# Optimization experiments

Measured on AMD Instinct MI355X. Metric: run time of the kernel, lower is better.

The kernel has to match this reference:

```python
import jax, jax.numpy as jnp
import numpy as np

N_NODES = 50000
N_EDGES = 800000
HIDDEN = 128
CONTEXT = 128


def setup_inputs() -> dict:
    key = jax.random.key(0)
    ks = jax.random.split(key, 8)
    s = 1.0 / np.sqrt(HIDDEN)
    return {
        "x": jax.random.normal(ks[0], (N_NODES, HIDDEN), jnp.float32),
        "edge_index": jax.random.randint(ks[1], (2, N_EDGES), 0, N_NODES, jnp.int64),
        "W_le": jax.random.normal(ks[2], (HIDDEN, 1), jnp.float32) * s,
        "b_le": jnp.zeros((1,), jnp.float32),
        "W1": jax.random.normal(ks[3], (HIDDEN, HIDDEN), jnp.float32) * s,
        "b1": jnp.zeros((HIDDEN,), jnp.float32),
        "W2": jax.random.normal(ks[4], (HIDDEN, CONTEXT), jnp.float32) * s,
        "b2": jnp.zeros((CONTEXT,), jnp.float32),
    }


def reference(x, edge_index, W_le, b_le, W1, b1, W2, b2):
    N = x.shape[0]
    src, dst = edge_index[0], edge_index[1]
    ar = jnp.arange(N)

    # leader election logits [N]
    logits = (x @ W_le + b_le)[:, 0]

    # extended edges with self loops (every destination segment non-empty)
    ext_src = jnp.concatenate([src, ar])
    ext_dst = jnp.concatenate([dst, ar])

    # scatter_max of source logits onto destinations; recover winning SOURCE node index
    val = logits[ext_src]                                   # [E+N]
    seg_max = jax.ops.segment_max(val, ext_dst, num_segments=N)  # [N]
    winner = jnp.where(val == seg_max[ext_dst], ext_src, -1)
    leader_idx = jax.ops.segment_max(winner, ext_dst, num_segments=N)  # [N] int
    is_leader = ar == leader_idx                            # [N] bool

    # scatter_mean of neighbor features onto destinations
    nsum = jax.ops.segment_sum(x[src], dst, num_segments=N)            # [N, H]
    cnt = jax.ops.segment_sum(jnp.ones((src.shape[0],), x.dtype), dst, num_segments=N)
    nmean = nsum / jnp.maximum(cnt, 1.0)[:, None]

    # squad report MLP (exact GELU, matching torch nn.GELU default)
    h = jax.nn.gelu(nmean @ W1 + b1, approximate=False)
    reports = h @ W2 + b2                                   # [N, C]
    all_reports = jnp.where(is_leader[:, None], reports, 0.0)

    # each node reads its leader's report
    squad_context = all_reports[leader_idx]                 # [N, C]
    return squad_context
```

## Files before the change

### kernel.cpp

```cpp
#include <hip/hip_runtime.h>
#include <stdint.h>

constexpr int NN  = 50000;
constexpr int NE  = 800000;
constexpr int H   = 128;
constexpr int CAP = 48;
constexpr int RB  = 8;

__device__ __forceinline__ uint32_t f32key(float f) {
  uint32_t b = __float_as_uint(f);
  return (b & 0x80000000u) ? ~b : (b | 0x80000000u);
}

__global__ void k_logits(const float* __restrict__ x,
                         const float* __restrict__ Wle, const float* __restrict__ ble,
                         float* __restrict__ logits, unsigned long long* __restrict__ lkey,
                         int* __restrict__ cnt, int* __restrict__ nsl) {
  int gid  = blockIdx.x * blockDim.x + threadIdx.x;
  int wave = gid >> 6, lane = threadIdx.x & 63;
  if (gid == 0) *nsl = 0;
  if (wave >= NN) return;
  const float* xr = x + (size_t)wave * H;
  float v = xr[lane] * Wle[lane] + xr[lane + 64] * Wle[lane + 64];
  for (int off = 32; off > 0; off >>= 1) v += __shfl_xor(v, off, 64);
  if (lane == 0) {
    float lg = v + ble[0];
    logits[wave] = lg;
    lkey[wave] = ((unsigned long long)f32key(lg) << 32) | (unsigned long long)(uint32_t)wave;
    cnt[wave] = 0;
  }
}

__global__ void k_elect(const int* __restrict__ esrc, const int* __restrict__ edst,
                        const float* __restrict__ logits, unsigned long long* __restrict__ lkey) {
  int e = blockIdx.x * blockDim.x + threadIdx.x;
  if (e >= NE) return;
  int s = __builtin_nontemporal_load(&esrc[e]);
  int d = __builtin_nontemporal_load(&edst[e]);
  unsigned long long key =
      ((unsigned long long)f32key(logits[s]) << 32) | (unsigned long long)(uint32_t)s;
  atomicMax(&lkey[d], key);
}

__global__ void k_place(const int* __restrict__ esrc, const int* __restrict__ edst,
                        const unsigned long long* __restrict__ lkey,
                        int* __restrict__ cnt, int* __restrict__ bucket,
                        int* __restrict__ slist, int* __restrict__ nsl) {
  const int* __restrict__ leader_lo = (const int*)lkey;
  int t = blockIdx.x * blockDim.x + threadIdx.x;
  if (t < NN) {
    if (leader_lo[2 * t] == t) {
      int p = atomicAdd(nsl, 1);
      slist[p] = t;
    }
  }
  if (t >= NE) return;
  int d = __builtin_nontemporal_load(&edst[t]);
  if (leader_lo[2 * d] != d) return;
  int s = esrc[t];
  int slot = atomicAdd(&cnt[d], 1);
  if (slot < CAP) bucket[(size_t)d * CAP + slot] = s;
}

__global__ void __launch_bounds__(256) k_report(
    const int* __restrict__ slist, const int* __restrict__ nsl,
    const int* __restrict__ cnt, const int* __restrict__ bucket,
    const float* __restrict__ x,
    const float* __restrict__ W1, const float* __restrict__ b1,
    const float* __restrict__ W2, const float* __restrict__ b2,
    float* __restrict__ out) {
  int base = blockIdx.x * RB;
  int ns = *nsl;
  if (base >= ns) return;
  int v = min(RB, ns - base);

  __shared__ float sm[RB][H];
  __shared__ float hm[RB][H];
  __shared__ int   ss[RB][CAP];
  __shared__ int   nodes[RB];
  __shared__ int   craw[RB];

  int tid = threadIdx.x;
  int j = tid & 127, half = tid >> 7;

  if (tid < RB) {
    int node = slist[base + min(tid, v - 1)];
    nodes[tid] = node;
    craw[tid] = cnt[node];
  }
  __syncthreads();
  for (int r = half; r < v; r += 2) {
    int cc = min(craw[r], CAP);
    if (j < cc) ss[r][j] = bucket[(size_t)nodes[r] * CAP + j];
  }
  __syncthreads();
  for (int rp = 0; rp < RB / 2; ++rp) {
    int r = 2 * rp + half;
    if (r >= v) break;
    int c = craw[r], cc = min(c, CAP);
    double a0 = 0.0, a1 = 0.0;
    int e = 0;
    for (; e + 1 < cc; e += 2) {
      a0 += (double)x[(size_t)ss[r][e] * H + j];
      a1 += (double)x[(size_t)ss[r][e + 1] * H + j];
    }
    if (e < cc) a0 += (double)x[(size_t)ss[r][e] * H + j];
    sm[r][j] = (float)(a0 + a1) * (1.0f / (float)max(c, 1));
  }
  __syncthreads();

  float acc[RB / 2];
#pragma unroll
  for (int rr = 0; rr < RB / 2; ++rr) acc[rr] = b1[j];
  for (int k = 0; k < H; ++k) {
    float w = W1[k * H + j];
#pragma unroll
    for (int rr = 0; rr < RB / 2; ++rr)
      acc[rr] = fmaf(sm[half * (RB / 2) + rr][k], w, acc[rr]);
  }
#pragma unroll
  for (int rr = 0; rr < RB / 2; ++rr)
    hm[half * (RB / 2) + rr][j] =
        0.5f * acc[rr] * (1.0f + erff(acc[rr] * 0.70710678118654752f));
  __syncthreads();

#pragma unroll
  for (int rr = 0; rr < RB / 2; ++rr) acc[rr] = b2[j];
  for (int k = 0; k < H; ++k) {
    float w = W2[k * H + j];
#pragma unroll
    for (int rr = 0; rr < RB / 2; ++rr)
      acc[rr] = fmaf(hm[half * (RB / 2) + rr][k], w, acc[rr]);
  }
#pragma unroll
  for (int rr = 0; rr < RB / 2; ++rr) {
    int r = half * (RB / 2) + rr;
    if (r < v)
      __builtin_nontemporal_store(acc[rr], &out[(size_t)nodes[r] * H + j]);
  }
}

__global__ void k_out(const unsigned long long* __restrict__ lkey,
                      float* __restrict__ out) {
  const int* __restrict__ leader_lo = (const int*)lkey;
  int g = blockIdx.x * blockDim.x + threadIdx.x;
  int i = g >> 5, q = g & 31;
  if (i >= NN) return;
  int L = leader_lo[2 * i];
  if (L == i) return;
  float4 v = make_float4(0.f, 0.f, 0.f, 0.f);
  if (leader_lo[2 * L] == L)
    v = *(const float4*)(out + (size_t)L * H + q * 4);
  float* o = out + (size_t)i * H + q * 4;
  __builtin_nontemporal_store(v.x, o + 0);
  __builtin_nontemporal_store(v.y, o + 1);
  __builtin_nontemporal_store(v.z, o + 2);
  __builtin_nontemporal_store(v.w, o + 3);
}

extern "C" void kernel_launch(void* const* d_in, const int* in_sizes, int n_in,
                              void* d_out, int out_size, void* d_ws, size_t ws_size,
                              hipStream_t stream) {
  (void)in_sizes; (void)n_in; (void)out_size; (void)ws_size;
  const float* x   = (const float*)d_in[0];
  const int* ei    = (const int*)d_in[1];
  const float* Wle = (const float*)d_in[2];
  const float* ble = (const float*)d_in[3];
  const float* W1  = (const float*)d_in[4];
  const float* b1  = (const float*)d_in[5];
  const float* W2  = (const float*)d_in[6];
  const float* b2  = (const float*)d_in[7];
  float* out       = (float*)d_out;

  char* ws = (char*)d_ws;
  unsigned long long* lkey = (unsigned long long*)ws;
  float* logits = (float*)(ws + 400000);
  int*   cnt    = (int*)  (ws + 600000);
  int*   slist  = (int*)  (ws + 800000);
  int*   nsl    = (int*)  (ws + 1000000);
  int*   bucket = (int*)  (ws + 1000256);

  const int* esrc = ei;
  const int* edst = ei + NE;

  k_logits<<<(NN * 64 + 255) / 256, 256, 0, stream>>>(x, Wle, ble, logits, lkey, cnt, nsl);
  k_elect<<<(NE + 255) / 256, 256, 0, stream>>>(esrc, edst, logits, lkey);
  k_place<<<(NE + 255) / 256, 256, 0, stream>>>(esrc, edst, lkey, cnt, bucket, slist, nsl);
  k_report<<<(NN + RB - 1) / RB, 256, 0, stream>>>(slist, nsl, cnt, bucket, x,
                                                   W1, b1, W2, b2, out);
  k_out<<<(NN * 32 + 255) / 256, 256, 0, stream>>>(lkey, out);
}
```

Before: 99.73 us.

## Fuse all stages into one persistent cooperative kernel with grid syncs

```diff
diff --git a/kernel.cpp b/kernel.cpp
--- a/kernel.cpp
+++ b/kernel.cpp
@@ -1,161 +1,180 @@
 #include <hip/hip_runtime.h>
+#include <hip/hip_cooperative_groups.h>
 #include <stdint.h>
+
+namespace cg = cooperative_groups;
 
 constexpr int NN  = 50000;
 constexpr int NE  = 800000;
 constexpr int H   = 128;
 constexpr int CAP = 48;
 constexpr int RB  = 8;
+constexpr int NBLK = 512;
+constexpr int NTHR = 256;
+constexpr int TOT  = NBLK * NTHR;
+
+typedef int vint4 __attribute__((ext_vector_type(4)));
 
 __device__ __forceinline__ uint32_t f32key(float f) {
   uint32_t b = __float_as_uint(f);
   return (b & 0x80000000u) ? ~b : (b | 0x80000000u);
 }
 
-__global__ void k_logits(const float* __restrict__ x,
-                         const float* __restrict__ Wle, const float* __restrict__ ble,
-                         float* __restrict__ logits, unsigned long long* __restrict__ lkey,
-                         int* __restrict__ cnt, int* __restrict__ nsl) {
-  int gid  = blockIdx.x * blockDim.x + threadIdx.x;
-  int wave = gid >> 6, lane = threadIdx.x & 63;
-  if (gid == 0) *nsl = 0;
-  if (wave >= NN) return;
-  const float* xr = x + (size_t)wave * H;
-  float v = xr[lane] * Wle[lane] + xr[lane + 64] * Wle[lane + 64];
-  for (int off = 32; off > 0; off >>= 1) v += __shfl_xor(v, off, 64);
-  if (lane == 0) {
-    float lg = v + ble[0];
-    logits[wave] = lg;
-    lkey[wave] = ((unsigned long long)f32key(lg) << 32) | (unsigned long long)(uint32_t)wave;
-    cnt[wave] = 0;
-  }
-}
-
-__global__ void k_elect(const int* __restrict__ esrc, const int* __restrict__ edst,
-                        const float* __restrict__ logits, unsigned long long* __restrict__ lkey) {
-  int e = blockIdx.x * blockDim.x + threadIdx.x;
-  if (e >= NE) return;
-  int s = __builtin_nontemporal_load(&esrc[e]);
-  int d = __builtin_nontemporal_load(&edst[e]);
-  unsigned long long key =
-      ((unsigned long long)f32key(logits[s]) << 32) | (unsigned long long)(uint32_t)s;
-  atomicMax(&lkey[d], key);
-}
-
-__global__ void k_place(const int* __restrict__ esrc, const int* __restrict__ edst,
-                        const unsigned long long* __restrict__ lkey,
-                        int* __restrict__ cnt, int* __restrict__ bucket,
-                        int* __restrict__ slist, int* __restrict__ nsl) {
-  const int* __restrict__ leader_lo = (const int*)lkey;
-  int t = blockIdx.x * blockDim.x + threadIdx.x;
-  if (t < NN) {
-    if (leader_lo[2 * t] == t) {
-      int p = atomicAdd(nsl, 1);
-      slist[p] = t;
-    }
-  }
-  if (t >= NE) return;
-  int d = __builtin_nontemporal_load(&edst[t]);
-  if (leader_lo[2 * d] != d) return;
-  int s = esrc[t];
-  int slot = atomicAdd(&cnt[d], 1);
-  if (slot < CAP) bucket[(size_t)d * CAP + slot] = s;
-}
-
-__global__ void __launch_bounds__(256) k_report(
-    const int* __restrict__ slist, const int* __restrict__ nsl,
-    const int* __restrict__ cnt, const int* __restrict__ bucket,
-    const float* __restrict__ x,
+__global__ void __launch_bounds__(NTHR, 2) k_all(
+    const float* __restrict__ x, const int* __restrict__ esrc, const int* __restrict__ edst,
+    const float* __restrict__ Wle, const float* __restrict__ ble,
     const float* __restrict__ W1, const float* __restrict__ b1,
     const float* __restrict__ W2, const float* __restrict__ b2,
-    float* __restrict__ out) {
-  int base = blockIdx.x * RB;
-  int ns = *nsl;
-  if (base >= ns) return;
-  int v = min(RB, ns - base);
+    unsigned long long* __restrict__ lkey, float* __restrict__ logits,
+    int* __restrict__ cnt, int* __restrict__ slist, int* __restrict__ nsl,
+    int* __restrict__ bucket, float* __restrict__ out) {
+  cg::grid_group grid = cg::this_grid();
+  const int tid = blockIdx.x * NTHR + threadIdx.x;
+  const int* __restrict__ leader_lo = (const int*)lkey;
 
   __shared__ float sm[RB][H];
   __shared__ float hm[RB][H];
   __shared__ int   ss[RB][CAP];
   __shared__ int   nodes[RB];
   __shared__ int   craw[RB];
-
-  int tid = threadIdx.x;
-  int j = tid & 127, half = tid >> 7;
-
-  if (tid < RB) {
-    int node = slist[base + min(tid, v - 1)];
-    nodes[tid] = node;
-    craw[tid] = cnt[node];
-  }
+  __shared__ int   ns_sh;
+
+  if (tid == 0) __builtin_nontemporal_store(0, nsl);
+  {
+    int gw = tid >> 6, lane = tid & 63;
+    for (int row = gw; row < NN; row += (TOT >> 6)) {
+      const float* xr = x + (size_t)row * H;
+      float v = xr[lane] * Wle[lane] + xr[lane + 64] * Wle[lane + 64];
+      for (int off = 32; off > 0; off >>= 1) v += __shfl_xor(v, off, 64);
+      if (lane == 0) {
+        float lg = v + ble[0];
+        __builtin_nontemporal_store(lg, &logits[row]);
+        unsigned long long sk =
+            ((unsigned long long)f32key(lg) << 32) | (unsigned long long)(uint32_t)row;
+        __builtin_nontemporal_store(sk, &lkey[row]);
+        __builtin_nontemporal_store(0, &cnt[row]);
+      }
+    }
+  }
+  grid.sync();
+
+  for (int g = tid; g < NE / 4; g += TOT) {
+    vint4 s4 = __builtin_nontemporal_load((const vint4*)esrc + g);
+    vint4 d4 = __builtin_nontemporal_load((const vint4*)edst + g);
+    float lg[4];
+#pragma unroll
+    for (int i = 0; i < 4; ++i) lg[i] = logits[s4[i]];
+#pragma unroll
+    for (int i = 0; i < 4; ++i) {
+      unsigned long long key =
+          ((unsigned long long)f32key(lg[i]) << 32) | (unsigned long long)(uint32_t)s4[i];
+      atomicMax(&lkey[d4[i]], key);
+    }
+  }
+  grid.sync();
+
+  for (int t = tid; t < NN; t += TOT) {
+    if (leader_lo[2 * t] == t) {
+      int p = atomicAdd(nsl, 1);
+      __builtin_nontemporal_store(t, &slist[p]);
+    }
+  }
+  for (int g = tid; g < NE / 4; g += TOT) {
+    vint4 d4 = __builtin_nontemporal_load((const vint4*)edst + g);
+    int L[4];
+#pragma unroll
+    for (int i = 0; i < 4; ++i) L[i] = leader_lo[2 * d4[i]];
+#pragma unroll
+    for (int i = 0; i < 4; ++i) {
+      if (L[i] == d4[i]) {
+        int s = esrc[g * 4 + i];
+        int slot = atomicAdd(&cnt[d4[i]], 1);
+        if (slot < CAP) __builtin_nontemporal_store(s, &bucket[(size_t)d4[i] * CAP + slot]);
+      }
+    }
+  }
+  grid.sync();
+
+  if (threadIdx.x == 0) ns_sh = atomicAdd(nsl, 0);
   __syncthreads();
-  for (int r = half; r < v; r += 2) {
-    int cc = min(craw[r], CAP);
-    if (j < cc) ss[r][j] = bucket[(size_t)nodes[r] * CAP + j];
-  }
-  __syncthreads();
-  for (int rp = 0; rp < RB / 2; ++rp) {
-    int r = 2 * rp + half;
-    if (r >= v) break;
-    int c = craw[r], cc = min(c, CAP);
-    double a0 = 0.0, a1 = 0.0;
-    int e = 0;
-    for (; e + 1 < cc; e += 2) {
-      a0 += (double)x[(size_t)ss[r][e] * H + j];
-      a1 += (double)x[(size_t)ss[r][e + 1] * H + j];
-    }
-    if (e < cc) a0 += (double)x[(size_t)ss[r][e] * H + j];
-    sm[r][j] = (float)(a0 + a1) * (1.0f / (float)max(c, 1));
-  }
-  __syncthreads();
-
-  float acc[RB / 2];
-#pragma unroll
-  for (int rr = 0; rr < RB / 2; ++rr) acc[rr] = b1[j];
-  for (int k = 0; k < H; ++k) {
-    float w = W1[k * H + j];
-#pragma unroll
-    for (int rr = 0; rr < RB / 2; ++rr)
-      acc[rr] = fmaf(sm[half * (RB / 2) + rr][k], w, acc[rr]);
-  }
-#pragma unroll
-  for (int rr = 0; rr < RB / 2; ++rr)
-    hm[half * (RB / 2) + rr][j] =
-        0.5f * acc[rr] * (1.0f + erff(acc[rr] * 0.70710678118654752f));
-  __syncthreads();
-
-#pragma unroll
-  for (int rr = 0; rr < RB / 2; ++rr) acc[rr] = b2[j];
-  for (int k = 0; k < H; ++k) {
-    float w = W2[k * H + j];
-#pragma unroll
-    for (int rr = 0; rr < RB / 2; ++rr)
-      acc[rr] = fmaf(hm[half * (RB / 2) + rr][k], w, acc[rr]);
-  }
-#pragma unroll
-  for (int rr = 0; rr < RB / 2; ++rr) {
-    int r = half * (RB / 2) + rr;
-    if (r < v)
-      __builtin_nontemporal_store(acc[rr], &out[(size_t)nodes[r] * H + j]);
-  }
-}
-
-__global__ void k_out(const unsigned long long* __restrict__ lkey,
-                      float* __restrict__ out) {
-  const int* __restrict__ leader_lo = (const int*)lkey;
-  int g = blockIdx.x * blockDim.x + threadIdx.x;
-  int i = g >> 5, q = g & 31;
-  if (i >= NN) return;
-  int L = leader_lo[2 * i];
-  if (L == i) return;
-  float4 v = make_float4(0.f, 0.f, 0.f, 0.f);
-  if (leader_lo[2 * L] == L)
-    v = *(const float4*)(out + (size_t)L * H + q * 4);
-  float* o = out + (size_t)i * H + q * 4;
-  __builtin_nontemporal_store(v.x, o + 0);
-  __builtin_nontemporal_store(v.y, o + 1);
-  __builtin_nontemporal_store(v.z, o + 2);
-  __builtin_nontemporal_store(v.w, o + 3);
+  const int ns = ns_sh;
+  {
+    int j = threadIdx.x & 127, half = threadIdx.x >> 7;
+    for (int base = blockIdx.x * RB; base < ns; base += NBLK * RB) {
+      int v = min(RB, ns - base);
+      if (threadIdx.x < RB) {
+        int node = slist[base + min((int)threadIdx.x, v - 1)];
+        nodes[threadIdx.x] = node;
+        craw[threadIdx.x] = cnt[node];
+      }
+      __syncthreads();
+      for (int r = half; r < v; r += 2) {
+        int cc = min(craw[r], CAP);
+        if (j < cc) ss[r][j] = bucket[(size_t)nodes[r] * CAP + j];
+      }
+      __syncthreads();
+      for (int rp = 0; rp < RB / 2; ++rp) {
+        int r = 2 * rp + half;
+        if (r >= v) break;
+        int c = craw[r], cc = min(c, CAP);
+        double a0 = 0.0, a1 = 0.0;
+        int e = 0;
+        for (; e + 1 < cc; e += 2) {
+          a0 += (double)x[(size_t)ss[r][e] * H + j];
+          a1 += (double)x[(size_t)ss[r][e + 1] * H + j];
+        }
+        if (e < cc) a0 += (double)x[(size_t)ss[r][e] * H + j];
+        sm[r][j] = (float)(a0 + a1) * (1.0f / (float)max(c, 1));
+      }
+      __syncthreads();
+
+      float acc[RB / 2];
+#pragma unroll
+      for (int rr = 0; rr < RB / 2; ++rr) acc[rr] = b1[j];
+      for (int k = 0; k < H; ++k) {
+        float w = W1[k * H + j];
+#pragma unroll
+        for (int rr = 0; rr < RB / 2; ++rr)
+          acc[rr] = fmaf(sm[half * (RB / 2) + rr][k], w, acc[rr]);
+      }
+#pragma unroll
+      for (int rr = 0; rr < RB / 2; ++rr)
+        hm[half * (RB / 2) + rr][j] =
+            0.5f * acc[rr] * (1.0f + erff(acc[rr] * 0.70710678118654752f));
+      __syncthreads();
+
+#pragma unroll
+      for (int rr = 0; rr < RB / 2; ++rr) acc[rr] = b2[j];
+      for (int k = 0; k < H; ++k) {
+        float w = W2[k * H + j];
+#pragma unroll
+        for (int rr = 0; rr < RB / 2; ++rr)
+          acc[rr] = fmaf(hm[half * (RB / 2) + rr][k], w, acc[rr]);
+      }
+#pragma unroll
+      for (int rr = 0; rr < RB / 2; ++rr) {
+        int r = half * (RB / 2) + rr;
+        if (r < v)
+          __builtin_nontemporal_store(acc[rr], &out[(size_t)nodes[r] * H + j]);
+      }
+      __syncthreads();
+    }
+  }
+  grid.sync();
+
+  for (int g = tid; g < NN * 32; g += TOT) {
+    int i = g >> 5, q = g & 31;
+    int L = leader_lo[2 * i];
+    if (L == i) continue;
+    float4 v = make_float4(0.f, 0.f, 0.f, 0.f);
+    if (leader_lo[2 * L] == L)
+      v = *(const float4*)(out + (size_t)L * H + q * 4);
+    float* o = out + (size_t)i * H + q * 4;
+    __builtin_nontemporal_store(v.x, o + 0);
+    __builtin_nontemporal_store(v.y, o + 1);
+    __builtin_nontemporal_store(v.z, o + 2);
+    __builtin_nontemporal_store(v.w, o + 3);
+  }
 }
 
 extern "C" void kernel_launch(void* const* d_in, const int* in_sizes, int n_in,
@@ -183,10 +202,9 @@
   const int* esrc = ei;
   const int* edst = ei + NE;
 
-  k_logits<<<(NN * 64 + 255) / 256, 256, 0, stream>>>(x, Wle, ble, logits, lkey, cnt, nsl);
-  k_elect<<<(NE + 255) / 256, 256, 0, stream>>>(esrc, edst, logits, lkey);
-  k_place<<<(NE + 255) / 256, 256, 0, stream>>>(esrc, edst, lkey, cnt, bucket, slist, nsl);
-  k_report<<<(NN + RB - 1) / RB, 256, 0, stream>>>(slist, nsl, cnt, bucket, x,
-                                                   W1, b1, W2, b2, out);
-  k_out<<<(NN * 32 + 255) / 256, 256, 0, stream>>>(lkey, out);
+  void* args[] = {(void*)&x, (void*)&esrc, (void*)&edst, (void*)&Wle, (void*)&ble,
+                  (void*)&W1, (void*)&b1, (void*)&W2, (void*)&b2,
+                  (void*)&lkey, (void*)&logits, (void*)&cnt, (void*)&slist,
+                  (void*)&nsl, (void*)&bucket, (void*)&out};
+  hipLaunchCooperativeKernel((const void*)k_all, dim3(NBLK), dim3(NTHR), args, 0, stream);
 }
```

New measurement: 336.2 us. 237% more time.

## Fuse edge bucketing into election pass and vectorize leader-report copy stores

Applied to the files above, without the earlier changes.

```diff
diff --git a/kernel.cpp b/kernel.cpp
--- a/kernel.cpp
+++ b/kernel.cpp
@@ -6,6 +6,8 @@
 constexpr int H   = 128;
 constexpr int CAP = 48;
 constexpr int RB  = 8;
+
+typedef float vfloat4 __attribute__((ext_vector_type(4)));
 
 __device__ __forceinline__ uint32_t f32key(float f) {
   uint32_t b = __float_as_uint(f);
@@ -31,8 +33,10 @@
   }
 }
 
-__global__ void k_elect(const int* __restrict__ esrc, const int* __restrict__ edst,
-                        const float* __restrict__ logits, unsigned long long* __restrict__ lkey) {
+__global__ void k_edge(const int* __restrict__ esrc, const int* __restrict__ edst,
+                       const float* __restrict__ logits,
+                       unsigned long long* __restrict__ lkey,
+                       int* __restrict__ cnt, int* __restrict__ bucket) {
   int e = blockIdx.x * blockDim.x + threadIdx.x;
   if (e >= NE) return;
   int s = __builtin_nontemporal_load(&esrc[e]);
@@ -40,26 +44,19 @@
   unsigned long long key =
       ((unsigned long long)f32key(logits[s]) << 32) | (unsigned long long)(uint32_t)s;
   atomicMax(&lkey[d], key);
+  int slot = atomicAdd(&cnt[d], 1);
+  if (slot < CAP) bucket[(size_t)d * CAP + slot] = s;
 }
 
-__global__ void k_place(const int* __restrict__ esrc, const int* __restrict__ edst,
-                        const unsigned long long* __restrict__ lkey,
-                        int* __restrict__ cnt, int* __restrict__ bucket,
+__global__ void k_slist(const unsigned long long* __restrict__ lkey,
                         int* __restrict__ slist, int* __restrict__ nsl) {
   const int* __restrict__ leader_lo = (const int*)lkey;
   int t = blockIdx.x * blockDim.x + threadIdx.x;
-  if (t < NN) {
-    if (leader_lo[2 * t] == t) {
-      int p = atomicAdd(nsl, 1);
-      slist[p] = t;
-    }
+  if (t >= NN) return;
+  if (leader_lo[2 * t] == t) {
+    int p = atomicAdd(nsl, 1);
+    slist[p] = t;
   }
-  if (t >= NE) return;
-  int d = __builtin_nontemporal_load(&edst[t]);
-  if (leader_lo[2 * d] != d) return;
-  int s = esrc[t];
-  int slot = atomicAdd(&cnt[d], 1);
-  if (slot < CAP) bucket[(size_t)d * CAP + slot] = s;
 }
 
 __global__ void __launch_bounds__(256) k_report(
@@ -148,14 +145,10 @@
   if (i >= NN) return;
   int L = leader_lo[2 * i];
   if (L == i) return;
-  float4 v = make_float4(0.f, 0.f, 0.f, 0.f);
+  vfloat4 v = {0.f, 0.f, 0.f, 0.f};
   if (leader_lo[2 * L] == L)
-    v = *(const float4*)(out + (size_t)L * H + q * 4);
-  float* o = out + (size_t)i * H + q * 4;
-  __builtin_nontemporal_store(v.x, o + 0);
-  __builtin_nontemporal_store(v.y, o + 1);
-  __builtin_nontemporal_store(v.z, o + 2);
-  __builtin_nontemporal_store(v.w, o + 3);
+    v = *(const vfloat4*)(out + (size_t)L * H + q * 4);
+  __builtin_nontemporal_store(v, (vfloat4*)(out + (size_t)i * H + q * 4));
 }
 
 extern "C" void kernel_launch(void* const* d_in, const int* in_sizes, int n_in,
@@ -184,8 +177,8 @@
   const int* edst = ei + NE;
 
   k_logits<<<(NN * 64 + 255) / 256, 256, 0, stream>>>(x, Wle, ble, logits, lkey, cnt, nsl);
-  k_elect<<<(NE + 255) / 256, 256, 0, stream>>>(esrc, edst, logits, lkey);
-  k_place<<<(NE + 255) / 256, 256, 0, stream>>>(esrc, edst, lkey, cnt, bucket, slist, nsl);
+  k_edge<<<(NE + 255) / 256, 256, 0, stream>>>(esrc, edst, logits, lkey, cnt, bucket);
+  k_slist<<<(NN + 255) / 256, 256, 0, stream>>>(lkey, slist, nsl);
   k_report<<<(NN + RB - 1) / RB, 256, 0, stream>>>(slist, nsl, cnt, bucket, x,
                                                    W1, b1, W2, b2, out);
   k_out<<<(NN * 32 + 255) / 256, 256, 0, stream>>>(lkey, out);
```

Result: slower. 131.7 us (+32.1%).
